# Kernel tuning notes

Hardware: AMD Instinct MI355X
Metric: run time of the kernel (lower is better)

Reference implementation:

```python
import jax, jax.numpy as jnp
import numpy as np

N_E = 8192
E_DIM = 256
BETA = 0.25

def setup_inputs() -> dict:
    key = jax.random.key(0)
    k1, k2 = jax.random.split(key)
    z = jax.random.normal(k1, (2, E_DIM, 8, 32, 32), dtype=jnp.float32)
    # nn.Embedding init: uniform(-1/n_e, 1/n_e)
    codebook = jax.random.uniform(k2, (N_E, E_DIM), dtype=jnp.float32,
                                  minval=-1.0 / N_E, maxval=1.0 / N_E)
    return {"z": z, "codebook": codebook}

def reference(z, codebook):
    # b c d h w -> b d h w c
    z_t = jnp.transpose(z, (0, 2, 3, 4, 1))  # [B,D,H,W,C]
    zf = z_t.reshape(-1, E_DIM)               # [N, C]
    # squared-distance: ||z||^2 + ||e||^2 - 2 z.e^T
    d = (jnp.sum(zf * zf, axis=1, keepdims=True)
         + jnp.sum(codebook * codebook, axis=1)
         - 2.0 * jnp.matmul(zf, codebook.T))  # [N, n_e]
    idx = jnp.argmin(d, axis=1)                # [N]
    z_q = codebook[idx].reshape(z_t.shape)     # [B,D,H,W,C]
    sg = jax.lax.stop_gradient
    loss = jnp.mean((sg(z_q) - z_t) ** 2) + BETA * jnp.mean((z_q - sg(z_t)) ** 2)
    # straight-through estimator
    z_q_st = z_t + sg(z_q - z_t)
    z_q_out = jnp.transpose(z_q_st, (0, 4, 1, 2, 3))  # [B,C,D,H,W]
    # perplexity (no-grad stats)
    min_encodings = jax.nn.one_hot(idx, N_E, dtype=jnp.float32)  # [N, n_e]
    e_mean = jnp.mean(min_encodings, axis=0)
    perplexity = jnp.exp(-jnp.sum(e_mean * jnp.log(e_mean + 1e-10)))
    return (z_q_out, loss, perplexity, min_encodings, idx)
```

## Files before the change

### kernel.cpp

```cpp
#include <hip/hip_runtime.h>

typedef _Float16 half8 __attribute__((ext_vector_type(8)));
typedef float floatx4 __attribute__((ext_vector_type(4)));

#define DEVI __device__ __forceinline__
#define AS1 __attribute__((address_space(1)))
#define AS3 __attribute__((address_space(3)))
#define GLL(gp, lp) __builtin_amdgcn_global_load_lds((const AS1 void*)(gp), (AS3 void*)(lp), 16, 0, 0)
#define VM6 asm volatile("s_waitcnt vmcnt(6)" ::: "memory")
#define VM8 asm volatile("s_waitcnt vmcnt(8)" ::: "memory")
#define VM2 asm volatile("s_waitcnt vmcnt(2)" ::: "memory")
#define BAR __builtin_amdgcn_s_barrier()

namespace {
constexpr int C_   = 256;
constexpr int DHW_ = 8192;
constexpr int N_   = 16384;
constexpr int NE_  = 8192;
constexpr int K_   = 256;

constexpr size_t LOSS_OFF  = 4194304;
constexpr size_t PERP_OFF  = 4194305;
constexpr size_t ENC_OFF   = 4194306;
constexpr size_t ENC_N     = 134217728ull;
constexpr size_t IDX_OFF   = ENC_OFF + ENC_N;

constexpr size_t SCR_ZH   = 480ull << 20;
constexpr size_t SCR_ZL   = 488ull << 20;
constexpr size_t SCR_EH   = 496ull << 20;
constexpr size_t SCR_EL   = 500ull << 20;
constexpr size_t SCR_ZZ   = 504ull << 20;
constexpr size_t SCR_KEY  = 505ull << 20;
constexpr size_t SCR_PART = 506ull << 20;
constexpr size_t SCR_HIST = 507ull << 20;

constexpr int NLOSS_BLOCKS = 2048;

constexpr size_t ZFILL_PER_BLK = 122880;
constexpr size_t TAIL_START    = 8 + 4096ull * ZFILL_PER_BLK;
constexpr size_t TAIL_F4       = (536870904ull - TAIL_START) / 16;
}


__global__ void vq_split(const float* __restrict__ z, const float* __restrict__ cb,
                         _Float16* __restrict__ ZHb, _Float16* __restrict__ ZLb,
                         _Float16* __restrict__ EHb, _Float16* __restrict__ ELb,
                         float* __restrict__ zz, unsigned long long* __restrict__ keys,
                         int* __restrict__ hist) {
    __shared__ float tile[64][260];
    int t = threadIdx.x;
    if (blockIdx.x < 512) {
        int n0 = blockIdx.x * 32;
        int b  = n0 >> 13;
        int d0 = n0 & 8191;
        const float* zb = z + (size_t)b * (C_ * DHW_) + d0;
        int j5 = t & 31, cg8 = t >> 5;
        for (int cc = 0; cc < 256; cc += 8) {
            int c = cc + cg8;
            tile[j5][c] = zb[(size_t)c * DHW_ + j5];
        }
        __syncthreads();
        int tl = n0 >> 8, r0 = n0 & 255;
        #pragma unroll
        for (int it = 0; it < 4; ++it) {
            int rid = it * 8 + cg8;
            half8 h, l;
            #pragma unroll
            for (int e = 0; e < 8; ++e) {
                float v = tile[j5][rid * 8 + e];
                _Float16 hh = (_Float16)v;
                h[e] = hh;
                l[e] = (_Float16)((v - (float)hh) * 2048.0f);
            }
            size_t off = ((size_t)(tl * 8 + (rid >> 2))) * 8192
                       + (size_t)(rid & 3) * 2048 + (size_t)(r0 + j5) * 8;
            *(half8*)(ZHb + off) = h;
            *(half8*)(ZLb + off) = l;
        }
        if (t < 32) {
            float tot[2];
            for (int h2 = 0; h2 < 2; ++h2) {
                float r8[8];
                #pragma unroll
                for (int k = 0; k < 8; ++k) { float x = tile[t][h2*128 + k]; r8[k] = x * x; }
                for (int i = 8; i < 128; i += 8) {
                    #pragma unroll
                    for (int k = 0; k < 8; ++k) { float x = tile[t][h2*128 + i + k]; r8[k] += x * x; }
                }
                tot[h2] = ((r8[0]+r8[1]) + (r8[2]+r8[3])) + ((r8[4]+r8[5]) + (r8[6]+r8[7]));
            }
            zz[n0 + t] = tot[0] + tot[1];
        }
        if (blockIdx.x < 64) keys[blockIdx.x * 256 + t] = ~0ull;
        else if (blockIdx.x < 96) hist[(blockIdx.x - 64) * 256 + t] = 0;
    } else {
        int j = t & 63, grp = t >> 6;
        int j0 = (blockIdx.x - 512) * 64;
        for (int i = 0; i < 64; ++i)
            tile[i][t] = cb[(size_t)(j0 + i) * K_ + t] * 65536.0f;
        __syncthreads();
        int tl = j0 >> 7, r0 = j0 & 127;
        #pragma unroll
        for (int it = 0; it < 8; ++it) {
            int rid = it * 4 + grp;
            half8 h, l;
            #pragma unroll
            for (int e = 0; e < 8; ++e) {
                float v = tile[j][rid * 8 + e];
                _Float16 hh = (_Float16)v;
                h[e] = hh;
                l[e] = (_Float16)((v - (float)hh) * 2048.0f);
            }
            size_t off = ((size_t)(tl * 8 + (rid >> 2))) * 4096
                       + (size_t)(rid & 3) * 1024 + (size_t)(r0 + j) * 8;
            *(half8*)(EHb + off) = h;
            *(half8*)(ELb + off) = l;
        }
    }
}


DEVI void stage_chunk(const char* zh, const char* zl, const char* eh, const char* el,
                      char* b, int t, int c) {
    #pragma unroll
    for (int i = 0; i < 2; ++i) {
        int f = i * 512 + t;
        int ao = (f >> 8) * 4096 + (f & 255) * 16;
        GLL(zh + (size_t)c * 16384 + ao, b + f * 16);
    }
    #pragma unroll
    for (int i = 0; i < 2; ++i) {
        int f = i * 512 + t;
        int ao = (f >> 8) * 4096 + (f & 255) * 16;
        GLL(zl + (size_t)c * 16384 + ao, b + 16384 + f * 16);
    }
    int eo = (t >> 7) * 2048 + (t & 127) * 16;
    GLL(eh + (size_t)c * 8192 + eo, b + 32768 + t * 16);
    GLL(el + (size_t)c * 8192 + eo, b + 40960 + t * 16);
}

DEVI void zfill2(char* zb, int t, int r0) {
    floatx4 z4 = {0.f, 0.f, 0.f, 0.f};
    __builtin_nontemporal_store(z4, (floatx4*)(zb + (size_t)r0 * 8192 + t * 16));
    __builtin_nontemporal_store(z4, (floatx4*)(zb + (size_t)(r0 + 1) * 8192 + t * 16));
}

DEVI void compute_chunk(const char* b, int wm, int wn, int g, int rr,
                        floatx4 (&acc_a)[4][4], floatx4 (&acc_b)[4][4]) {
    const char* Ab = b + g * 4096;
    const char* Bb = b + 32768 + g * 2048;
    half8 azh[4], azl[4], beh[4], bel[4];
    #pragma unroll
    for (int f = 0; f < 4; ++f) {
        int row = wm * 64 + f * 16 + rr;
        azh[f] = *(const half8*)(Ab + row * 16);
        azl[f] = *(const half8*)(Ab + 16384 + row * 16);
        int col = wn * 64 + f * 16 + rr;
        beh[f] = *(const half8*)(Bb + col * 16);
        bel[f] = *(const half8*)(Bb + 8192 + col * 16);
    }
    __builtin_amdgcn_s_setprio(1);
    #pragma unroll
    for (int fi = 0; fi < 4; ++fi)
        #pragma unroll
        for (int fj = 0; fj < 4; ++fj) {
            acc_a[fi][fj] = __builtin_amdgcn_mfma_f32_16x16x32_f16(azh[fi], beh[fj], acc_a[fi][fj], 0, 0, 0);
            acc_b[fi][fj] = __builtin_amdgcn_mfma_f32_16x16x32_f16(azl[fi], beh[fj], acc_b[fi][fj], 0, 0, 0);
            acc_b[fi][fj] = __builtin_amdgcn_mfma_f32_16x16x32_f16(azh[fi], bel[fj], acc_b[fi][fj], 0, 0, 0);
        }
    __builtin_amdgcn_s_setprio(0);
}

__launch_bounds__(512, 2)
__global__ void vq_gemm_argmin(const _Float16* __restrict__ ZHb, const _Float16* __restrict__ ZLb,
                               const _Float16* __restrict__ EHb, const _Float16* __restrict__ ELb,
                               const float* __restrict__ zz,
                               unsigned long long* __restrict__ keys,
                               char* __restrict__ zfill) {
    __shared__ _Float16 lds[3][24576];
    __shared__ unsigned long long rowmin[256];

    int orig = blockIdx.x;
    int xcd = orig & 7;
    int loc = orig >> 3;
    int bm = xcd * 8 + (loc & 7);
    int bn = loc >> 3;
    int m0 = bm * 256, n0v = bn * 128;

    int t = threadIdx.x;
    int lane = t & 63, wid = t >> 6;
    int wm = wid >> 1, wn = wid & 1;
    int g = lane >> 4, rr = lane & 15;

    const char* zh = (const char*)ZHb + (size_t)bm * 131072;
    const char* zl = (const char*)ZLb + (size_t)bm * 131072;
    const char* eh = (const char*)EHb + (size_t)bn * 65536;
    const char* el = (const char*)ELb + (size_t)bn * 65536;
    char* zb = zfill + (size_t)orig * ZFILL_PER_BLK;

    floatx4 acc_a[4][4], acc_b[4][4];
    #pragma unroll
    for (int i = 0; i < 4; ++i)
        #pragma unroll
        for (int jj = 0; jj < 4; ++jj) {
            acc_a[i][jj] = (floatx4){0.f, 0.f, 0.f, 0.f};
            acc_b[i][jj] = (floatx4){0.f, 0.f, 0.f, 0.f};
        }

    char* L0 = (char*)lds[0];
    char* L1 = (char*)lds[1];
    char* L2 = (char*)lds[2];

    stage_chunk(zh, zl, eh, el, L0, t, 0);
    stage_chunk(zh, zl, eh, el, L1, t, 1);
    VM6; BAR;
    stage_chunk(zh, zl, eh, el, L2, t, 2); zfill2(zb, t, 0);  compute_chunk(L0, wm, wn, g, rr, acc_a, acc_b); VM8; BAR;
    stage_chunk(zh, zl, eh, el, L0, t, 3); zfill2(zb, t, 2);  compute_chunk(L1, wm, wn, g, rr, acc_a, acc_b); VM8; BAR;
    stage_chunk(zh, zl, eh, el, L1, t, 4); zfill2(zb, t, 4);  compute_chunk(L2, wm, wn, g, rr, acc_a, acc_b); VM8; BAR;
    stage_chunk(zh, zl, eh, el, L2, t, 5); zfill2(zb, t, 6);  compute_chunk(L0, wm, wn, g, rr, acc_a, acc_b); VM8; BAR;
    stage_chunk(zh, zl, eh, el, L0, t, 6); zfill2(zb, t, 8);  compute_chunk(L1, wm, wn, g, rr, acc_a, acc_b); VM8; BAR;
    stage_chunk(zh, zl, eh, el, L1, t, 7); zfill2(zb, t, 10); compute_chunk(L2, wm, wn, g, rr, acc_a, acc_b); VM8; BAR;
    zfill2(zb, t, 12);                                        compute_chunk(L0, wm, wn, g, rr, acc_a, acc_b); VM2; BAR;
    {
        floatx4 z4 = {0.f, 0.f, 0.f, 0.f};
        __builtin_nontemporal_store(z4, (floatx4*)(zb + 14ull * 8192 + t * 16));
    }
    compute_chunk(L1, wm, wn, g, rr, acc_a, acc_b);

    if (t < 256) rowmin[t] = ~0ull;
    __syncthreads();

    constexpr float S_A = 1.0f / 65536.0f;
    constexpr float S_B = 1.0f / 134217728.0f;
    #pragma unroll
    for (int fi = 0; fi < 4; ++fi) {
        #pragma unroll
        for (int r = 0; r < 4; ++r) {
            int rowl = wm * 64 + fi * 16 + g * 4 + r;
            float zzv = zz[m0 + rowl];
            unsigned long long best = ~0ull;
            #pragma unroll
            for (int fj = 0; fj < 4; ++fj) {
                float dot = acc_a[fi][fj][r] * S_A + acc_b[fi][fj][r] * S_B;
                float d = zzv - 2.0f * dot;
                unsigned int db = __float_as_uint(d);
                unsigned int jg = (unsigned)(n0v + wn * 64 + fj * 16 + rr);
                unsigned long long key = ((unsigned long long)db << 32) | jg;
                if (key < best) best = key;
            }
            #pragma unroll
            for (int s = 1; s < 16; s <<= 1) {
                unsigned long long o = __shfl_xor(best, s, 64);
                if (o < best) best = o;
            }
            if (rr == 0) atomicMin(&rowmin[rowl], best);
        }
    }
    __syncthreads();
    if (t < 256) atomicMin(&keys[m0 + t], rowmin[t]);
}

__global__ void vq_zq_loss(const float* __restrict__ z, const float* __restrict__ cb,
                           const unsigned long long* __restrict__ keys,
                           float* __restrict__ out0, float* __restrict__ parts,
                           float* __restrict__ out_idx, int* __restrict__ hist) {
    size_t i0 = ((size_t)blockIdx.x * 256 + threadIdx.x) * 8;
    int c   = (int)((i0 >> 13) & 255);
    int b   = (int)(i0 >> 21);
    int dhw = (int)(i0 & 8191);
    int nb  = b * DHW_ + dhw;
    int jj[8];
    #pragma unroll
    for (int e = 0; e < 8; ++e)
        jj[e] = (int)(unsigned)(keys[nb + e] & 0xFFFFFFFFull);
    float ls = 0.f;
    #pragma unroll
    for (int e = 0; e < 8; ++e) {
        float zq = cb[(size_t)jj[e] * K_ + c];
        float zt = z[i0 + e];
        float diff = zq - zt;
        out0[i0 + e] = zt + diff;
        ls += diff * diff;
    }
    if (c == 0) {
        #pragma unroll
        for (int e = 0; e < 8; ++e) {
            out_idx[nb + e] = (float)jj[e];
            atomicAdd(&hist[jj[e]], 1);
        }
    }
    __shared__ float red[256];
    red[threadIdx.x] = ls;
    __syncthreads();
    for (int s = 128; s > 0; s >>= 1) {
        if (threadIdx.x < (unsigned)s) red[threadIdx.x] += red[threadIdx.x + s];
        __syncthreads();
    }
    if (threadIdx.x == 0) parts[blockIdx.x] = red[0];
}

__global__ void vq_finalize_scalars(const float* __restrict__ parts,
                                    const int* __restrict__ hist,
                                    float* __restrict__ out) {
    __shared__ double dred[256];
    int t = threadIdx.x;
    double ent = 0.0;
    for (int i = t; i < NE_; i += 256) {
        float em = (float)hist[i] * (1.0f / 16384.0f);
        float term = em * logf(em + 1e-10f);
        ent += (double)term;
    }
    dred[t] = ent;
    __syncthreads();
    for (int s = 128; s > 0; s >>= 1) {
        if (t < s) dred[t] += dred[t + s];
        __syncthreads();
    }
    double entr = 0.0;
    if (t == 0) entr = dred[0];
    __syncthreads();
    double ls = 0.0;
    for (int i = t; i < NLOSS_BLOCKS; i += 256) ls += (double)parts[i];
    dred[t] = ls;
    __syncthreads();
    for (int s = 128; s > 0; s >>= 1) {
        if (t < s) dred[t] += dred[t + s];
        __syncthreads();
    }
    if (t == 0) {
        double m = dred[0] / 4194304.0;
        float m1 = (float)m;
        out[LOSS_OFF] = m1 + 0.25f * m1;
        out[PERP_OFF] = (float)exp(-entr);
    }
}

__global__ void vq_zero_tail(char* __restrict__ encb) {
    size_t i = (size_t)blockIdx.x * 256 + threadIdx.x;
    floatx4 z4 = {0.f, 0.f, 0.f, 0.f};
    char* base = encb + TAIL_START;
    for (size_t k = i; k < TAIL_F4; k += 131072)
        *(floatx4*)(base + k * 16) = z4;
    if (i == 0) {
        float2 z2 = {0.f, 0.f};
        *(float2*)encb = z2;
        *(float2*)(encb + 536870904ull) = z2;
    }
}

__global__ void vq_write_ones(const float* __restrict__ idxf, float* __restrict__ enc) {
    int n = blockIdx.x * 256 + threadIdx.x;
    enc[(size_t)n * NE_ + (int)idxf[n]] = 1.0f;
}

extern "C" void kernel_launch(void* const* d_in, const int* in_sizes, int n_in,
                              void* d_out, int out_size, void* d_ws, size_t ws_size,
                              hipStream_t stream) {
    const float* z  = (const float*)d_in[0];
    const float* cb = (const float*)d_in[1];
    float* out = (float*)d_out;

    char* scr = (char*)(((uintptr_t)(out + ENC_OFF) + 255) & ~(uintptr_t)255);
    _Float16* ZHb = (_Float16*)(scr + SCR_ZH);
    _Float16* ZLb = (_Float16*)(scr + SCR_ZL);
    _Float16* EHb = (_Float16*)(scr + SCR_EH);
    _Float16* ELb = (_Float16*)(scr + SCR_EL);
    float* zz = (float*)(scr + SCR_ZZ);
    unsigned long long* keys = (unsigned long long*)(scr + SCR_KEY);
    float* parts = (float*)(scr + SCR_PART);
    int* hist = (int*)(scr + SCR_HIST);
    float* out_idx = out + IDX_OFF;
    float* enc = out + ENC_OFF;
    char* encb = (char*)enc;

    vq_split<<<640, 256, 0, stream>>>(z, cb, ZHb, ZLb, EHb, ELb, zz, keys, hist);
    vq_gemm_argmin<<<4096, 512, 0, stream>>>(ZHb, ZLb, EHb, ELb, zz, keys, encb + 8);
    vq_zq_loss<<<NLOSS_BLOCKS, 256, 0, stream>>>(z, cb, keys, out, parts, out_idx, hist);
    vq_finalize_scalars<<<1, 256, 0, stream>>>(parts, hist, out);
    vq_zero_tail<<<512, 256, 0, stream>>>(encb);
    vq_write_ones<<<64, 256, 0, stream>>>(out_idx, enc);
}
```

Measured before the change: 291.9 us.

## Split each GEMM chunk into two barrier-separated MFMA phases interleaved with staging

Each K-chunk's compute is split into two halves over the codebook columns. The global-to-LDS loads (high parts, then low parts) and the zero-fill stores are issued between the halves, with explicit barriers, lgkmcnt waits and sched_barriers fencing each MFMA cluster. The goal is a finer-grained, ping-pong style interleave of memory issue and matrix work, and lower register pressure from holding only half the B fragments at a time. In exchange it doubles the barriers per chunk and depends on hand-tuned vmcnt values; the last chunk's wait template has no case for 2, so no wait is emitted there.

```diff
diff --git a/kernel.cpp b/kernel.cpp
--- a/kernel.cpp
+++ b/kernel.cpp
@@ -7,10 +7,9 @@
 #define AS1 __attribute__((address_space(1)))
 #define AS3 __attribute__((address_space(3)))
 #define GLL(gp, lp) __builtin_amdgcn_global_load_lds((const AS1 void*)(gp), (AS3 void*)(lp), 16, 0, 0)
-#define VM6 asm volatile("s_waitcnt vmcnt(6)" ::: "memory")
-#define VM8 asm volatile("s_waitcnt vmcnt(8)" ::: "memory")
-#define VM2 asm volatile("s_waitcnt vmcnt(2)" ::: "memory")
 #define BAR __builtin_amdgcn_s_barrier()
+#define LGKM0 asm volatile("s_waitcnt lgkmcnt(0)" ::: "memory")
+#define MFMA16(a, b, c) __builtin_amdgcn_mfma_f32_16x16x32_f16(a, b, c, 0, 0, 0)
 
 namespace {
 constexpr int C_   = 256;
@@ -120,55 +119,104 @@
 }
 
 
-DEVI void stage_chunk(const char* zh, const char* zl, const char* eh, const char* el,
-                      char* b, int t, int c) {
-    #pragma unroll
-    for (int i = 0; i < 2; ++i) {
-        int f = i * 512 + t;
-        int ao = (f >> 8) * 4096 + (f & 255) * 16;
-        GLL(zh + (size_t)c * 16384 + ao, b + f * 16);
-    }
-    #pragma unroll
-    for (int i = 0; i < 2; ++i) {
-        int f = i * 512 + t;
-        int ao = (f >> 8) * 4096 + (f & 255) * 16;
-        GLL(zl + (size_t)c * 16384 + ao, b + 16384 + f * 16);
-    }
-    int eo = (t >> 7) * 2048 + (t & 127) * 16;
-    GLL(eh + (size_t)c * 8192 + eo, b + 32768 + t * 16);
-    GLL(el + (size_t)c * 8192 + eo, b + 40960 + t * 16);
-}
-
-DEVI void zfill2(char* zb, int t, int r0) {
+template<int N> DEVI void vmwait() {
+    if constexpr (N == 9) asm volatile("s_waitcnt vmcnt(9)" ::: "memory");
+    else if constexpr (N == 8) asm volatile("s_waitcnt vmcnt(8)" ::: "memory");
+    else if constexpr (N == 6) asm volatile("s_waitcnt vmcnt(6)" ::: "memory");
+    else if constexpr (N == 3) asm volatile("s_waitcnt vmcnt(3)" ::: "memory");
+    else if constexpr (N == 0) asm volatile("s_waitcnt vmcnt(0)" ::: "memory");
+}
+
+template<int HALF>
+DEVI void stage_half(const char* zh, const char* zl, const char* eh, const char* el,
+                     char* b, int t, int c) {
+    if constexpr (HALF == 0) {
+        #pragma unroll
+        for (int i = 0; i < 2; ++i) {
+            int f = i * 512 + t;
+            int ao = (f >> 8) * 4096 + (f & 255) * 16;
+            GLL(zh + (size_t)c * 16384 + ao, b + f * 16);
+        }
+        int eo = (t >> 7) * 2048 + (t & 127) * 16;
+        GLL(eh + (size_t)c * 8192 + eo, b + 32768 + t * 16);
+    } else {
+        #pragma unroll
+        for (int i = 0; i < 2; ++i) {
+            int f = i * 512 + t;
+            int ao = (f >> 8) * 4096 + (f & 255) * 16;
+            GLL(zl + (size_t)c * 16384 + ao, b + 16384 + f * 16);
+        }
+        int eo = (t >> 7) * 2048 + (t & 127) * 16;
+        GLL(el + (size_t)c * 8192 + eo, b + 40960 + t * 16);
+    }
+}
+
+DEVI void ntz(char* zb, int t, int r0) {
     floatx4 z4 = {0.f, 0.f, 0.f, 0.f};
     __builtin_nontemporal_store(z4, (floatx4*)(zb + (size_t)r0 * 8192 + t * 16));
-    __builtin_nontemporal_store(z4, (floatx4*)(zb + (size_t)(r0 + 1) * 8192 + t * 16));
-}
-
-DEVI void compute_chunk(const char* b, int wm, int wn, int g, int rr,
-                        floatx4 (&acc_a)[4][4], floatx4 (&acc_b)[4][4]) {
-    const char* Ab = b + g * 4096;
-    const char* Bb = b + 32768 + g * 2048;
-    half8 azh[4], azl[4], beh[4], bel[4];
+}
+
+template<int VMN, bool STG, bool NT1, bool NT2>
+DEVI void do_chunk(const char* cur, char* stg, int cs,
+                   const char* zh, const char* zl, const char* eh, const char* el,
+                   char* zb, int zr0,
+                   int wm, int wn, int g, int rr, int t,
+                   floatx4 (&acc_a)[4][4], floatx4 (&acc_b)[4][4]) {
+    const char* Ab = cur + g * 4096;
+    const char* Bb = cur + 32768 + g * 2048;
+    half8 azh[4], azl[4], beh[2], bel[2];
     #pragma unroll
     for (int f = 0; f < 4; ++f) {
         int row = wm * 64 + f * 16 + rr;
         azh[f] = *(const half8*)(Ab + row * 16);
         azl[f] = *(const half8*)(Ab + 16384 + row * 16);
+    }
+    #pragma unroll
+    for (int f = 0; f < 2; ++f) {
         int col = wn * 64 + f * 16 + rr;
         beh[f] = *(const half8*)(Bb + col * 16);
         bel[f] = *(const half8*)(Bb + 8192 + col * 16);
     }
+    if constexpr (STG) stage_half<0>(zh, zl, eh, el, stg, t, cs);
+    if constexpr (NT1) ntz(zb, t, zr0);
+    BAR;
+    LGKM0;
+    __builtin_amdgcn_sched_barrier(0);
     __builtin_amdgcn_s_setprio(1);
     #pragma unroll
     for (int fi = 0; fi < 4; ++fi)
         #pragma unroll
-        for (int fj = 0; fj < 4; ++fj) {
-            acc_a[fi][fj] = __builtin_amdgcn_mfma_f32_16x16x32_f16(azh[fi], beh[fj], acc_a[fi][fj], 0, 0, 0);
-            acc_b[fi][fj] = __builtin_amdgcn_mfma_f32_16x16x32_f16(azl[fi], beh[fj], acc_b[fi][fj], 0, 0, 0);
-            acc_b[fi][fj] = __builtin_amdgcn_mfma_f32_16x16x32_f16(azh[fi], bel[fj], acc_b[fi][fj], 0, 0, 0);
+        for (int fj = 0; fj < 2; ++fj) {
+            acc_a[fi][fj] = MFMA16(azh[fi], beh[fj], acc_a[fi][fj]);
+            acc_b[fi][fj] = MFMA16(azl[fi], beh[fj], acc_b[fi][fj]);
+            acc_b[fi][fj] = MFMA16(azh[fi], bel[fj], acc_b[fi][fj]);
         }
     __builtin_amdgcn_s_setprio(0);
+    BAR;
+    half8 beh2[2], bel2[2];
+    #pragma unroll
+    for (int f = 0; f < 2; ++f) {
+        int col = wn * 64 + (f + 2) * 16 + rr;
+        beh2[f] = *(const half8*)(Bb + col * 16);
+        bel2[f] = *(const half8*)(Bb + 8192 + col * 16);
+    }
+    if constexpr (STG) stage_half<1>(zh, zl, eh, el, stg, t, cs);
+    if constexpr (NT2) ntz(zb, t, zr0 + 1);
+    vmwait<VMN>();
+    BAR;
+    LGKM0;
+    __builtin_amdgcn_sched_barrier(0);
+    __builtin_amdgcn_s_setprio(1);
+    #pragma unroll
+    for (int fi = 0; fi < 4; ++fi)
+        #pragma unroll
+        for (int fj = 0; fj < 2; ++fj) {
+            acc_a[fi][fj + 2] = MFMA16(azh[fi], beh2[fj], acc_a[fi][fj + 2]);
+            acc_b[fi][fj + 2] = MFMA16(azl[fi], beh2[fj], acc_b[fi][fj + 2]);
+            acc_b[fi][fj + 2] = MFMA16(azh[fi], bel2[fj], acc_b[fi][fj + 2]);
+        }
+    __builtin_amdgcn_s_setprio(0);
+    BAR;
 }
 
 __launch_bounds__(512, 2)
@@ -211,21 +259,18 @@
     char* L1 = (char*)lds[1];
     char* L2 = (char*)lds[2];
 
-    stage_chunk(zh, zl, eh, el, L0, t, 0);
-    stage_chunk(zh, zl, eh, el, L1, t, 1);
-    VM6; BAR;
-    stage_chunk(zh, zl, eh, el, L2, t, 2); zfill2(zb, t, 0);  compute_chunk(L0, wm, wn, g, rr, acc_a, acc_b); VM8; BAR;
-    stage_chunk(zh, zl, eh, el, L0, t, 3); zfill2(zb, t, 2);  compute_chunk(L1, wm, wn, g, rr, acc_a, acc_b); VM8; BAR;
-    stage_chunk(zh, zl, eh, el, L1, t, 4); zfill2(zb, t, 4);  compute_chunk(L2, wm, wn, g, rr, acc_a, acc_b); VM8; BAR;
-    stage_chunk(zh, zl, eh, el, L2, t, 5); zfill2(zb, t, 6);  compute_chunk(L0, wm, wn, g, rr, acc_a, acc_b); VM8; BAR;
-    stage_chunk(zh, zl, eh, el, L0, t, 6); zfill2(zb, t, 8);  compute_chunk(L1, wm, wn, g, rr, acc_a, acc_b); VM8; BAR;
-    stage_chunk(zh, zl, eh, el, L1, t, 7); zfill2(zb, t, 10); compute_chunk(L2, wm, wn, g, rr, acc_a, acc_b); VM8; BAR;
-    zfill2(zb, t, 12);                                        compute_chunk(L0, wm, wn, g, rr, acc_a, acc_b); VM2; BAR;
-    {
-        floatx4 z4 = {0.f, 0.f, 0.f, 0.f};
-        __builtin_nontemporal_store(z4, (floatx4*)(zb + 14ull * 8192 + t * 16));
-    }
-    compute_chunk(L1, wm, wn, g, rr, acc_a, acc_b);
+    stage_half<0>(zh, zl, eh, el, L0, t, 0); stage_half<1>(zh, zl, eh, el, L0, t, 0);
+    stage_half<0>(zh, zl, eh, el, L1, t, 1); stage_half<1>(zh, zl, eh, el, L1, t, 1);
+    vmwait<6>(); BAR;
+
+    do_chunk<8, true,  true, true >(L0, L2, 2, zh, zl, eh, el, zb, 0,  wm, wn, g, rr, t, acc_a, acc_b);
+    do_chunk<9, true,  true, true >(L1, L0, 3, zh, zl, eh, el, zb, 2,  wm, wn, g, rr, t, acc_a, acc_b);
+    do_chunk<9, true,  true, true >(L2, L1, 4, zh, zl, eh, el, zb, 4,  wm, wn, g, rr, t, acc_a, acc_b);
+    do_chunk<9, true,  true, true >(L0, L2, 5, zh, zl, eh, el, zb, 6,  wm, wn, g, rr, t, acc_a, acc_b);
+    do_chunk<9, true,  true, true >(L1, L0, 6, zh, zl, eh, el, zb, 8,  wm, wn, g, rr, t, acc_a, acc_b);
+    do_chunk<9, true,  true, true >(L2, L1, 7, zh, zl, eh, el, zb, 10, wm, wn, g, rr, t, acc_a, acc_b);
+    do_chunk<3, false, true, true >(L0, L0, 0, zh, zl, eh, el, zb, 12, wm, wn, g, rr, t, acc_a, acc_b);
+    do_chunk<2, false, true, false>(L1, L1, 0, zh, zl, eh, el, zb, 14, wm, wn, g, rr, t, acc_a, acc_b);
 
     if (t < 256) rowmin[t] = ~0ull;
     __syncthreads();
```

Result: slower. 299.7 us (+2.7%).
